# Kernel optimization log

Measured on AMD Instinct MI355X. Metric: run time of the kernel, lower is better.

Reference implementation:

```python
import jax, jax.numpy as jnp
import numpy as np

B, D_IN, T = 16, 512, 4096
N_CB, K, D_CB = 9, 1024, 8
EPS = 1e-12  # F.normalize eps


def setup_inputs() -> dict:
    key = jax.random.key(0)
    ks = jax.random.split(key, 8)
    z = jax.random.normal(ks[0], (B, D_IN, T), dtype=jnp.float32)
    # weight-norm params: weight = g * v / ||v|| (norm over all dims except out-channel)
    in_v = jax.random.normal(ks[1], (N_CB, D_CB, D_IN), dtype=jnp.float32) * 0.05
    in_g = jax.random.uniform(ks[2], (N_CB, D_CB), minval=0.5, maxval=1.5, dtype=jnp.float32)
    in_b = jax.random.normal(ks[3], (N_CB, D_CB), dtype=jnp.float32) * 0.01
    out_v = jax.random.normal(ks[4], (N_CB, D_IN, D_CB), dtype=jnp.float32) * 0.05
    out_g = jax.random.uniform(ks[5], (N_CB, D_IN), minval=0.5, maxval=1.5, dtype=jnp.float32)
    out_b = jax.random.normal(ks[6], (N_CB, D_IN), dtype=jnp.float32) * 0.01
    codebooks = jax.random.normal(ks[7], (N_CB, K, D_CB), dtype=jnp.float32)
    return dict(z=z, in_v=in_v, in_g=in_g, in_b=in_b,
                out_v=out_v, out_g=out_g, out_b=out_b, codebooks=codebooks)


def _wn_weight(g, v):
    # weight_norm over dim=0: normalize each output row of v
    return g[:, None] * v / jnp.linalg.norm(v, axis=1, keepdims=True)


def reference(z, in_v, in_g, in_b, out_v, out_g, out_b, codebooks):
    def step(carry, p):
        residual, latent, closs, bloss = carry
        ivi, igi, ibi, ovi, ogi, obi, cb = p
        # in_proj (1x1 conv == channel matmul)
        W_in = _wn_weight(igi, ivi)                               # [d_cb, d_in]
        z_e = jnp.einsum('oc,bct->bot', W_in, residual) + ibi[None, :, None]  # [b, d_cb, t]
        enc = z_e.transpose(0, 2, 1).reshape(B * T, D_CB)         # (b t) d
        enc_n = enc / jnp.maximum(jnp.linalg.norm(enc, axis=1, keepdims=True), EPS)
        cb_n = cb / jnp.maximum(jnp.linalg.norm(cb, axis=1, keepdims=True), EPS)
        # squared L2 distance between normalized vectors
        dist = ((enc_n * enc_n).sum(1, keepdims=True)
                - 2.0 * enc_n @ cb_n.T
                + (cb_n * cb_n).sum(1)[None, :])                  # [(b t), K]
        idx = jnp.argmin(dist, axis=1).reshape(B, T)              # [b, t]
        z_q = cb[idx].transpose(0, 2, 1)                          # [b, d_cb, t] (raw codebook)
        # losses: per-batch mean over [1,2], then mean over batch == global mean (eval mask all True)
        closs = closs + ((z_e - jax.lax.stop_gradient(z_q)) ** 2).mean()
        bloss = bloss + ((z_q - jax.lax.stop_gradient(z_e)) ** 2).mean()
        # straight-through estimator
        z_q_st = z_e + jax.lax.stop_gradient(z_q - z_e)
        W_out = _wn_weight(ogi, ovi)                              # [d_in, d_cb]
        lat_i = jnp.einsum('oc,bct->bot', W_out, z_q_st) + obi[None, :, None]  # [b, d_in, t]
        latent = latent + lat_i
        residual = residual - lat_i
        return (residual, latent, closs, bloss), idx

    init = (z, jnp.zeros_like(z), jnp.float32(0.0), jnp.float32(0.0))
    xs = (in_v, in_g, in_b, out_v, out_g, out_b, codebooks)
    (_, latent, closs, bloss), indices = jax.lax.scan(step, init, xs)
    codes = indices.transpose(1, 0, 2)  # [b, n_codebooks, t]
    return codes, latent, closs, bloss
```

## Files before the change

### kernel.cpp

```cpp
#include <hip/hip_runtime.h>
#include <hip/hip_bf16.h>

constexpr int NB  = 16;
constexpr int DIN = 512;
constexpr int TT  = 4096;
constexpr int NCB = 9;
constexpr int KK  = 1024;

constexpr size_t OUT_LAT   = (size_t)NB * NCB * TT;
constexpr size_t OUT_CLOSS = OUT_LAT + (size_t)NB * DIN * TT;

constexpr int SRES = 514;
constexpr int SWIN = 516;

__device__ __align__(16) float g_cbn [NCB * KK * 8];
__device__ __align__(16) float g_c2  [NCB * KK];
__device__ __align__(16) float g_win [NCB * 8 * DIN];
__device__ __align__(16) float g_wout[NCB * DIN * 8];
__device__ __align__(16) float g_obt [NCB * DIN];
__device__ double g_loss;

__device__ __forceinline__ float sqf(float x) {
  float r = x * x;
  asm volatile("" : "+v"(r));
  return r;
}

__global__ void prep_win_k(const float* __restrict__ in_v, const float* __restrict__ in_g) {
  const int r = blockIdx.x * 64 + threadIdx.x;
  if (r >= NCB * 8) return;
  const float* v = in_v + (size_t)r * DIN;
  float blk[4];
#pragma unroll
  for (int bb = 0; bb < 4; ++bb) {
    const float* a = v + bb * 128;
    float r8[8];
#pragma unroll
    for (int j = 0; j < 8; ++j) r8[j] = sqf(a[j]);
#pragma unroll
    for (int m = 1; m < 16; ++m)
#pragma unroll
      for (int j = 0; j < 8; ++j) r8[j] += sqf(a[m * 8 + j]);
    blk[bb] = ((r8[0] + r8[1]) + (r8[2] + r8[3])) + ((r8[4] + r8[5]) + (r8[6] + r8[7]));
  }
  const float total = (blk[0] + blk[1]) + (blk[2] + blk[3]);
  const float nrm = sqrtf(total);
  const float g = in_g[r];
  float* w = g_win + (size_t)r * DIN;
  for (int c = 0; c < DIN; ++c) w[c] = (g * v[c]) / nrm;
}

__global__ void prep_wout_k(const float* __restrict__ out_v, const float* __restrict__ out_g,
                            const float* __restrict__ out_b) {
  const int row = blockIdx.x * 256 + threadIdx.x;
  const float* v = out_v + (size_t)row * 8;
  float q[8];
#pragma unroll
  for (int d = 0; d < 8; ++d) q[d] = sqf(v[d]);
  const float nrm = sqrtf(((q[0] + q[1]) + (q[2] + q[3])) + ((q[4] + q[5]) + (q[6] + q[7])));
  const float g = out_g[row];
  const int i = row >> 9, c = row & 511;
  float* w = g_wout + (((size_t)i * 32 + (c & 31)) * 16 + (c >> 5)) * 8;
#pragma unroll
  for (int d = 0; d < 8; ++d) w[d] = (g * v[d]) / nrm;
  g_obt[((size_t)i * 32 + (c & 31)) * 16 + (c >> 5)] = out_b[row];
}

__global__ void prep_cbn_k(const float* __restrict__ cb) {
  const int row = blockIdx.x * 256 + threadIdx.x;
  const float* v = cb + (size_t)row * 8;
  float q[8];
#pragma unroll
  for (int d = 0; d < 8; ++d) q[d] = sqf(v[d]);
  float nrm = sqrtf(((q[0] + q[1]) + (q[2] + q[3])) + ((q[4] + q[5]) + (q[6] + q[7])));
  nrm = fmaxf(nrm, 1e-12f);
  const int i = row >> 10, k = row & 1023;
  float* dst = g_cbn + (((size_t)i * 32 + (k & 31)) * 32 + (k >> 5)) * 8;
  float cn[8];
#pragma unroll
  for (int d = 0; d < 8; ++d) { cn[d] = v[d] / nrm; dst[d] = cn[d]; }
  float s2[8];
#pragma unroll
  for (int d = 0; d < 8; ++d) s2[d] = sqf(cn[d]);
  g_c2[(size_t)i * 1024 + (k & 31) * 32 + (k >> 5)] =
      ((s2[0] + s2[1]) + (s2[2] + s2[3])) + ((s2[4] + s2[5]) + (s2[6] + s2[7]));
  if (row == 0) g_loss = 0.0;
}

__global__ __launch_bounds__(512, 4)
void rvq_main_k(const float* __restrict__ z, const float* __restrict__ in_b,
                const float* __restrict__ cb, float* __restrict__ out) {
  __shared__ __align__(16) float s_res[16 * SRES];
  __shared__ __align__(16) float s_win[8 * SWIN];
  __shared__ float s_ze[128];
  __shared__ float s_en[128];
  __shared__ float s_s[16];
  __shared__ float s_cd[128];
  __shared__ int   s_ck[128];

  const int tid = threadIdx.x;
  const int col = tid & 15;
  const int grp = tid >> 4;
  const int b   = blockIdx.x >> 8;
  const int t0  = (blockIdx.x & 255) << 4;

  float lr[16];
  {
    const float* zb = z + (size_t)b * DIN * TT + t0 + col;
#pragma unroll
    for (int j = 0; j < 16; ++j) {
      const int c = grp + (j << 5);
      s_res[col * SRES + c] = zb[(size_t)c * TT];
      lr[j] = 0.0f;
    }
  }

  float loss_acc = 0.0f;

  for (int i = 0; i < NCB; ++i) {
    {
      const float4* gw = (const float4*)(g_win + i * 4096);
#pragma unroll
      for (int q = 0; q < 2; ++q) {
        const int e = (q * 512 + tid) * 4;
        *(float4*)(s_win + (e >> 9) * SWIN + (e & 511)) = gw[q * 512 + tid];
      }
    }
    __syncthreads();

    if (tid < 128) {
      const int a_col = tid >> 3, a_o = tid & 7;
      const float2* wr = (const float2*)(s_win + a_o * SWIN);
      const float2* rr = (const float2*)(s_res + a_col * SRES);
      float acc = 0.0f;
#pragma unroll 8
      for (int h = 0; h < 256; ++h) {
        const float2 w = wr[h];
        const float2 r = rr[h];
        acc = fmaf(w.x, r.x, acc);
        acc = fmaf(w.y, r.y, acc);
      }
      const float ze = acc + in_b[i * 8 + a_o];
      s_ze[a_o * 16 + a_col] = ze;
      const float q = sqf(ze);
      const float t1 = q + __shfl_xor(q, 1);
      const float t2 = t1 + __shfl_xor(t1, 2);
      const float t3 = t2 + __shfl_xor(t2, 4);
      float nrm = sqrtf(t3);
      nrm = fmaxf(nrm, 1e-12f);
      const float en = ze / nrm;
      s_en[a_o * 16 + a_col] = en;
      const float s2 = sqf(en);
      const float u1 = s2 + __shfl_xor(s2, 1);
      const float u2 = u1 + __shfl_xor(u1, 2);
      const float u3 = u2 + __shfl_xor(u2, 4);
      if (a_o == 0) s_s[a_col] = u3;
    }
    __syncthreads();

    {
      const float en0 = s_en[col],      en1 = s_en[16 + col];
      const float en2 = s_en[32 + col], en3 = s_en[48 + col];
      const float en4 = s_en[64 + col], en5 = s_en[80 + col];
      const float en6 = s_en[96 + col], en7 = s_en[112 + col];
      const float sv = s_s[col];
      const float* cp  = g_cbn + ((size_t)i * 32 + grp) * 256;
      const float* c2p = g_c2  + (size_t)i * 1024 + grp * 32;
      float dmin = 3.402823466e38f; int jmin = 0;
      for (int jo = 0; jo < 8; ++jo) {
        const float4 c2q = *(const float4*)(c2p + jo * 4);
        const float c2a[4] = {c2q.x, c2q.y, c2q.z, c2q.w};
#pragma unroll
        for (int ji = 0; ji < 4; ++ji) {
          const int j = jo * 4 + ji;
          const float4 c0 = *(const float4*)(cp + j * 8);
          const float4 c1 = *(const float4*)(cp + j * 8 + 4);
          float dot = 0.0f;
          dot = fmaf(en0, c0.x, dot); dot = fmaf(en1, c0.y, dot);
          dot = fmaf(en2, c0.z, dot); dot = fmaf(en3, c0.w, dot);
          dot = fmaf(en4, c1.x, dot); dot = fmaf(en5, c1.y, dot);
          dot = fmaf(en6, c1.z, dot); dot = fmaf(en7, c1.w, dot);
          const float dist = fmaf(-2.0f, dot, sv) + c2a[ji];
          if (dist < dmin) { dmin = dist; jmin = j; }
        }
      }
      int kmin = (jmin << 5) + grp;
      float od = __shfl_xor(dmin, 16); int ok = __shfl_xor(kmin, 16);
      if (od < dmin || (od == dmin && ok < kmin)) { dmin = od; kmin = ok; }
      od = __shfl_xor(dmin, 32); ok = __shfl_xor(kmin, 32);
      if (od < dmin || (od == dmin && ok < kmin)) { dmin = od; kmin = ok; }
      if ((tid & 48) == 0) {
        s_cd[(tid >> 6) * 16 + col] = dmin;
        s_ck[(tid >> 6) * 16 + col] = kmin;
      }
    }
    __syncthreads();

    {
      float bd = s_cd[col]; int bk = s_ck[col];
#pragma unroll
      for (int w = 1; w < 8; ++w) {
        const float d2 = s_cd[w * 16 + col]; const int k2 = s_ck[w * 16 + col];
        if (d2 < bd || (d2 == bd && k2 < bk)) { bd = d2; bk = k2; }
      }
      if (grp == 0)
        out[((size_t)b * NCB + i) * TT + t0 + col] = (float)bk;

      const float* cr = cb + ((size_t)i * KK + bk) * 8;
      const float4 cq0 = *(const float4*)(cr);
      const float4 cq1 = *(const float4*)(cr + 4);
      const float zqa[8] = {cq0.x, cq0.y, cq0.z, cq0.w, cq1.x, cq1.y, cq1.z, cq1.w};
      float qst[8];
#pragma unroll
      for (int d = 0; d < 8; ++d) {
        const float ze = s_ze[d * 16 + col];
        const float zq = zqa[d];
        qst[d] = ze + (zq - ze);
        if (grp == 0) {
          const float df = ze - zq;
          loss_acc = fmaf(df, df, loss_acc);
        }
      }
      const float* gw  = g_wout + ((size_t)i * 32 + grp) * 128;
      const float* obp = g_obt  + (size_t)i * 512 + grp * 16;
      for (int jo = 0; jo < 4; ++jo) {
        const float4 obq = *(const float4*)(obp + jo * 4);
        const float oba[4] = {obq.x, obq.y, obq.z, obq.w};
#pragma unroll
        for (int ji = 0; ji < 4; ++ji) {
          const int j = jo * 4 + ji;
          const float4 w0 = *(const float4*)(gw + j * 8);
          const float4 w1 = *(const float4*)(gw + j * 8 + 4);
          float dot = 0.0f;
          dot = fmaf(w0.x, qst[0], dot); dot = fmaf(w0.y, qst[1], dot);
          dot = fmaf(w0.z, qst[2], dot); dot = fmaf(w0.w, qst[3], dot);
          dot = fmaf(w1.x, qst[4], dot); dot = fmaf(w1.y, qst[5], dot);
          dot = fmaf(w1.z, qst[6], dot); dot = fmaf(w1.w, qst[7], dot);
          const float lat = dot + oba[ji];
          lr[j] += lat;
          s_res[col * SRES + grp + (j << 5)] -= lat;
        }
      }
    }
  }

  {
    float* lat = out + OUT_LAT;
#pragma unroll
    for (int j = 0; j < 16; ++j) {
      const int c = grp + (j << 5);
      lat[((size_t)b * DIN + c) * TT + t0 + col] = lr[j];
    }
  }

  if (tid < 64) {
    float v = loss_acc;
#pragma unroll
    for (int off = 32; off; off >>= 1) v += __shfl_down(v, off);
    if (tid == 0) atomicAdd(&g_loss, (double)v);
  }
}

__global__ void rvq_epi_k(float* __restrict__ out) {
  const float m = (float)(g_loss / 524288.0);
  out[OUT_CLOSS]     = m;
  out[OUT_CLOSS + 1] = m;
}

extern "C" void kernel_launch(void* const* d_in, const int* in_sizes, int n_in,
                              void* d_out, int out_size, void* d_ws, size_t ws_size,
                              hipStream_t stream) {
  const float* z     = (const float*)d_in[0];
  const float* in_v  = (const float*)d_in[1];
  const float* in_g  = (const float*)d_in[2];
  const float* in_b  = (const float*)d_in[3];
  const float* out_v = (const float*)d_in[4];
  const float* out_g = (const float*)d_in[5];
  const float* out_b = (const float*)d_in[6];
  const float* cb    = (const float*)d_in[7];
  float* out = (float*)d_out;
  (void)d_ws; (void)ws_size;

  prep_win_k <<<2, 64, 0, stream>>>(in_v, in_g);
  prep_wout_k<<<18, 256, 0, stream>>>(out_v, out_g, out_b);
  prep_cbn_k <<<36, 256, 0, stream>>>(cb);
  rvq_main_k <<<4096, 512, 0, stream>>>(z, in_b, cb, out);
  rvq_epi_k  <<<1, 1, 0, stream>>>(out);
}
```

Before: 1.494 ms.

## Stage codebook and projection weights in LDS, prefetch next in_proj weights

Each stage's normalized codebook, squared norms, out-projection weights and biases are now copied into shared memory by the 384 threads that sit idle during the in-projection. Those threads also prefetch the next stage's in-projection weights into a double-buffered LDS slot, so the loads overlap with compute. The goal is to replace repeated global/L2 reads in the argmin and out-projection loops with LDS reads. The cost is much more LDS per block, and launch bounds drop from 4 to 2 blocks per CU, which reduces occupancy.

Result: no change. 1.510 ms (+1.1%).

```diff
diff --git a/kernel.cpp b/kernel.cpp
--- a/kernel.cpp
+++ b/kernel.cpp
@@ -12,6 +12,10 @@
 
 constexpr int SRES = 514;
 constexpr int SWIN = 516;
+constexpr int SCBN = 260;
+constexpr int SC2  = 36;
+constexpr int SWO  = 132;
+constexpr int SOB  = 20;
 
 __device__ __align__(16) float g_cbn [NCB * KK * 8];
 __device__ __align__(16) float g_c2  [NCB * KK];
@@ -87,11 +91,15 @@
   if (row == 0) g_loss = 0.0;
 }
 
-__global__ __launch_bounds__(512, 4)
+__global__ __launch_bounds__(512, 2)
 void rvq_main_k(const float* __restrict__ z, const float* __restrict__ in_b,
                 const float* __restrict__ cb, float* __restrict__ out) {
-  __shared__ __align__(16) float s_res[16 * SRES];
-  __shared__ __align__(16) float s_win[8 * SWIN];
+  __shared__ __align__(16) float s_res [16 * SRES];
+  __shared__ __align__(16) float s_win [2 * 8 * SWIN];
+  __shared__ __align__(16) float s_cbn [32 * SCBN];
+  __shared__ __align__(16) float s_c2  [32 * SC2];
+  __shared__ __align__(16) float s_wout[32 * SWO];
+  __shared__ __align__(16) float s_obt [32 * SOB];
   __shared__ float s_ze[128];
   __shared__ float s_en[128];
   __shared__ float s_s[16];
@@ -114,23 +122,24 @@
       lr[j] = 0.0f;
     }
   }
+  {
+    const float4* src = (const float4*)(g_win);
+#pragma unroll
+    for (int r = 0; r < 2; ++r) {
+      const int idx = tid + r * 512;
+      const int row = idx >> 7, off = idx & 127;
+      *(float4*)(s_win + row * SWIN + off * 4) = src[idx];
+    }
+  }
 
   float loss_acc = 0.0f;
 
   for (int i = 0; i < NCB; ++i) {
-    {
-      const float4* gw = (const float4*)(g_win + i * 4096);
-#pragma unroll
-      for (int q = 0; q < 2; ++q) {
-        const int e = (q * 512 + tid) * 4;
-        *(float4*)(s_win + (e >> 9) * SWIN + (e & 511)) = gw[q * 512 + tid];
-      }
-    }
     __syncthreads();
 
     if (tid < 128) {
       const int a_col = tid >> 3, a_o = tid & 7;
-      const float2* wr = (const float2*)(s_win + a_o * SWIN);
+      const float2* wr = (const float2*)(s_win + (i & 1) * (8 * SWIN) + a_o * SWIN);
       const float2* rr = (const float2*)(s_res + a_col * SRES);
       float acc = 0.0f;
 #pragma unroll 8
@@ -155,6 +164,52 @@
       const float u2 = u1 + __shfl_xor(u1, 2);
       const float u3 = u2 + __shfl_xor(u2, 4);
       if (a_o == 0) s_s[a_col] = u3;
+    } else {
+      const int st = tid - 128;
+      {
+        const float4* src = (const float4*)(g_cbn + (size_t)i * (KK * 8));
+#pragma unroll
+        for (int r = 0; r < 6; ++r) {
+          const int idx = st + r * 384;
+          if (idx < 2048) {
+            const int row = idx >> 6, off = idx & 63;
+            *(float4*)(s_cbn + row * SCBN + off * 4) = src[idx];
+          }
+        }
+      }
+      if (st < 256) {
+        const float4* src = (const float4*)(g_c2 + (size_t)i * KK);
+        const int row = st >> 3, off = st & 7;
+        *(float4*)(s_c2 + row * SC2 + off * 4) = src[st];
+      }
+      {
+        const float4* src = (const float4*)(g_wout + (size_t)i * (DIN * 8));
+#pragma unroll
+        for (int r = 0; r < 3; ++r) {
+          const int idx = st + r * 384;
+          if (idx < 1024) {
+            const int row = idx >> 5, off = idx & 31;
+            *(float4*)(s_wout + row * SWO + off * 4) = src[idx];
+          }
+        }
+      }
+      if (st < 128) {
+        const float4* src = (const float4*)(g_obt + (size_t)i * DIN);
+        const int row = st >> 2, off = st & 3;
+        *(float4*)(s_obt + row * SOB + off * 4) = src[st];
+      }
+      if (i + 1 < NCB) {
+        const float4* src = (const float4*)(g_win + (size_t)(i + 1) * (8 * DIN));
+        float* dstb = s_win + ((i + 1) & 1) * (8 * SWIN);
+#pragma unroll
+        for (int r = 0; r < 3; ++r) {
+          const int idx = st + r * 384;
+          if (idx < 1024) {
+            const int row = idx >> 7, off = idx & 127;
+            *(float4*)(dstb + row * SWIN + off * 4) = src[idx];
+          }
+        }
+      }
     }
     __syncthreads();
 
@@ -164,8 +219,8 @@
       const float en4 = s_en[64 + col], en5 = s_en[80 + col];
       const float en6 = s_en[96 + col], en7 = s_en[112 + col];
       const float sv = s_s[col];
-      const float* cp  = g_cbn + ((size_t)i * 32 + grp) * 256;
-      const float* c2p = g_c2  + (size_t)i * 1024 + grp * 32;
+      const float* cp  = s_cbn + grp * SCBN;
+      const float* c2p = s_c2  + grp * SC2;
       float dmin = 3.402823466e38f; int jmin = 0;
       for (int jo = 0; jo < 8; ++jo) {
         const float4 c2q = *(const float4*)(c2p + jo * 4);
@@ -221,8 +276,8 @@
           loss_acc = fmaf(df, df, loss_acc);
         }
       }
-      const float* gw  = g_wout + ((size_t)i * 32 + grp) * 128;
-      const float* obp = g_obt  + (size_t)i * 512 + grp * 16;
+      const float* gw  = s_wout + grp * SWO;
+      const float* obp = s_obt  + grp * SOB;
       for (int jo = 0; jo < 4; ++jo) {
         const float4 obq = *(const float4*)(obp + jo * 4);
         const float oba[4] = {obq.x, obq.y, obq.z, obq.w};
```
